# Performance work log

Measured on AMD Instinct MI355X. Metric: run time of the kernel, lower is better.

## Reference

```python
import jax, jax.numpy as jnp
import numpy as np

N_NODES = 100000
N_EDGES = 3200000
N_GRAPHS = 2048
D_IN = 128
D_H = 128
D_OUT = 2
BN_EPS = 1e-5


def setup_inputs() -> dict:
    key = jax.random.key(0)
    ks = jax.random.split(key, 24)
    x = jax.random.normal(ks[0], (N_NODES, D_IN), dtype=jnp.float32)
    edge_index = jax.random.randint(ks[1], (2, N_EDGES), 0, N_NODES, dtype=jnp.int64)
    batch = jnp.sort(jax.random.randint(ks[2], (N_NODES,), 0, N_GRAPHS, dtype=jnp.int64))

    def lin(k, din, dout):
        return jax.random.normal(k, (din, dout), dtype=jnp.float32) / np.sqrt(din)

    inp = {
        'x': x, 'edge_index': edge_index, 'batch': batch,
        'W1': lin(ks[3], D_IN, D_H), 'b1': jnp.zeros((D_H,), jnp.float32),
        'W2': lin(ks[4], D_H, D_H), 'b2': jnp.zeros((D_H,), jnp.float32),
        'W3': lin(ks[5], D_H, D_H), 'b3': jnp.zeros((D_H,), jnp.float32),
    }
    for i, kk in zip((1, 2, 3), (ks[6], ks[7], ks[8])):
        inp[f'bn{i}_g'] = 1.0 + 0.1 * jax.random.normal(jax.random.fold_in(kk, 0), (D_H,), jnp.float32)
        inp[f'bn{i}_b'] = 0.1 * jax.random.normal(jax.random.fold_in(kk, 1), (D_H,), jnp.float32)
        inp[f'bn{i}_m'] = 0.1 * jax.random.normal(jax.random.fold_in(kk, 2), (D_H,), jnp.float32)
        inp[f'bn{i}_v'] = 0.5 + jax.random.uniform(jax.random.fold_in(kk, 3), (D_H,), jnp.float32)
    inp['fc1_W'] = lin(ks[9], D_H, D_H)
    inp['fc1_b'] = jnp.zeros((D_H,), jnp.float32)
    inp['fc2_W'] = lin(ks[10], D_H, D_OUT)
    inp['fc2_b'] = jnp.zeros((D_OUT,), jnp.float32)
    return inp


def _gcn_conv(x, W, b, src, dst, dinv):
    # h = X W, then out[dst] += (dinv[src]*dinv[dst]) * h[src]  (self-loops already in src/dst)
    h = x @ W
    norm = dinv[src] * dinv[dst]  # [E+N]
    msg = h[src] * norm[:, None]  # [E+N, D]
    out = jax.ops.segment_sum(msg, dst, num_segments=N_NODES)
    return out + b


def _bn_eval(x, g, b, m, v):
    return (x - m) * (g * jax.lax.rsqrt(v + BN_EPS)) + b


def reference(x, edge_index, batch, W1, b1, W2, b2, W3, b3,
              bn1_g, bn1_b, bn1_m, bn1_v, bn2_g, bn2_b, bn2_m, bn2_v,
              bn3_g, bn3_b, bn3_m, bn3_v, fc1_W, fc1_b, fc2_W, fc2_b):
    loops = jnp.arange(N_NODES, dtype=edge_index.dtype)
    src = jnp.concatenate([edge_index[0], loops])
    dst = jnp.concatenate([edge_index[1], loops])
    deg = jax.ops.segment_sum(jnp.ones_like(dst, dtype=x.dtype), dst, num_segments=N_NODES)
    dinv = jnp.where(deg > 0, jax.lax.rsqrt(jnp.maximum(deg, 1.0)), 0.0)

    h = jax.nn.relu(_bn_eval(_gcn_conv(x, W1, b1, src, dst, dinv), bn1_g, bn1_b, bn1_m, bn1_v))
    h = jax.nn.relu(_bn_eval(_gcn_conv(h, W2, b2, src, dst, dinv), bn2_g, bn2_b, bn2_m, bn2_v))
    h = jax.nn.relu(_bn_eval(_gcn_conv(h, W3, b3, src, dst, dinv), bn3_g, bn3_b, bn3_m, bn3_v))

    # global mean pool over graphs
    sums = jax.ops.segment_sum(h, batch, num_segments=N_GRAPHS)
    cnts = jax.ops.segment_sum(jnp.ones((N_NODES,), h.dtype), batch, num_segments=N_GRAPHS)
    pooled = sums / jnp.maximum(cnts, 1.0)[:, None]  # [G, D_H]

    z = jax.nn.relu(pooled @ fc1_W + fc1_b)
    logits = z @ fc2_W + fc2_b
    return jax.nn.log_softmax(logits, axis=1)
```

## Files before the change

kernel.cpp:

```cpp
#include <hip/hip_runtime.h>
#include <stdint.h>

#define NN 100000
#define NE 3200000
#define NG 2048
#define DH 128

#define NBUK 196
#define BSH 9
#define BMASK 511
#define BUKCAP 18200
#define EPT 16
#define EPW 4096

#define WLROW 136

typedef __attribute__((ext_vector_type(8))) short v8s;
typedef __attribute__((ext_vector_type(4))) float v4f;
typedef __attribute__((ext_vector_type(2))) float f2;

__device__ __forceinline__ float bf2f(unsigned short u) {
  union { unsigned int i; float f; } v; v.i = ((unsigned int)u) << 16; return v.f;
}
__device__ __forceinline__ unsigned short f2bf(float f) {
  union { float f; unsigned int i; } v; v.f = f;
  unsigned int i = v.i;
  unsigned int r = (i + 0x7FFFu + ((i >> 16) & 1u)) >> 16;
  return (unsigned short)r;
}
__device__ __forceinline__ int eload(const void* p, long long i, int is64) {
  return is64 ? (int)((const long long*)p)[i] : ((const int*)p)[i];
}
__device__ __forceinline__ float pload(const void* p, int i, int isbf) {
  return isbf ? bf2f(((const unsigned short*)p)[i]) : ((const float*)p)[i];
}
__device__ __forceinline__ void upadd2(unsigned int w, f2& acc) {
  union { unsigned int u; float f; } a, b;
  a.u = w << 16; b.u = w & 0xffff0000u;
  f2 u; u.x = a.f; u.y = b.f;
  acc += u;
}
#define ACC4(v) do { upadd2((v).x, a01); upadd2((v).y, a23); \
                     upadd2((v).z, a45); upadd2((v).w, a67); } while (0)

__device__ __forceinline__ void gather_row(const uint4* Hc, const int* colv,
    int beg, int end, int q, f2& a01, f2& a23, f2& a45, f2& a67) {
  int j = beg;
  for (; j + 32 <= end; j += 32) {
    int s0 = colv[j + q],      s1 = colv[j + 4 + q];
    int s2 = colv[j + 8 + q],  s3 = colv[j + 12 + q];
    int s4 = colv[j + 16 + q], s5 = colv[j + 20 + q];
    int s6 = colv[j + 24 + q], s7 = colv[j + 28 + q];
    uint4 v0 = Hc[s0 * 16]; uint4 v1 = Hc[s1 * 16];
    uint4 v2 = Hc[s2 * 16]; uint4 v3 = Hc[s3 * 16];
    uint4 v4 = Hc[s4 * 16]; uint4 v5 = Hc[s5 * 16];
    uint4 v6 = Hc[s6 * 16]; uint4 v7 = Hc[s7 * 16];
    ACC4(v0); ACC4(v1); ACC4(v2); ACC4(v3);
    ACC4(v4); ACC4(v5); ACC4(v6); ACC4(v7);
  }
  for (; j + 16 <= end; j += 16) {
    int s0 = colv[j + q],     s1 = colv[j + 4 + q];
    int s2 = colv[j + 8 + q], s3 = colv[j + 12 + q];
    uint4 v0 = Hc[s0 * 16]; uint4 v1 = Hc[s1 * 16];
    uint4 v2 = Hc[s2 * 16]; uint4 v3 = Hc[s3 * 16];
    ACC4(v0); ACC4(v1); ACC4(v2); ACC4(v3);
  }
  for (; j + 4 <= end; j += 4) {
    uint4 v0 = Hc[colv[j + q] * 16];
    ACC4(v0);
  }
  if (j + q < end) {
    uint4 v0 = Hc[colv[j + q] * 16];
    ACC4(v0);
  }
}

constexpr size_t al(size_t x) { return (x + 255) & ~size_t(255); }
constexpr size_t OFF_FLAGS = 0;
constexpr size_t OFF_DINV  = 256;
constexpr size_t OFF_ROWP  = al(OFF_DINV + 4ull * NN);
constexpr size_t OFF_GSTART= al(OFF_ROWP + 4ull * (NN + 1));
constexpr size_t OFF_BCUR  = al(OFF_GSTART + 4ull * (NG + 1));
constexpr size_t OFF_WT    = al(OFF_BCUR + 1024);
constexpr size_t OFF_FC1W  = al(OFF_WT + 2ull * 3 * 16384);
constexpr size_t OFF_FC2W  = al(OFF_FC1W + 4ull * 16384);
constexpr size_t OFF_PVEC  = al(OFF_FC2W + 4ull * 256);
constexpr size_t OFF_AC    = al(OFF_PVEC + 4ull * 17 * 128);
constexpr size_t OFF_COL   = al(OFF_AC + 4ull * 768);
constexpr size_t OFF_H     = al(OFF_COL + 4ull * NE);
constexpr size_t OFF_Y     = al(OFF_H + 2ull * NN * 128);
constexpr size_t WS_NEED   = OFF_Y + 2ull * NN * 128;
constexpr size_t OFF_REC   = OFF_H;


__global__ __launch_bounds__(256) void probe_k(const void* edge, const void* batch,
                                               const void* x, int* flags, int* bcur) {
  __shared__ int cnt_e, cnt_b, cnt_f;
  int t = threadIdx.x;
  bcur[t] = 0;
  if (t == 0) { cnt_e = 0; cnt_b = 0; cnt_f = 0; }
  __syncthreads();
  int le = 0, lb = 0, lf = 0;
  for (int i = t; i < 512; i += 256) {
    uint2 p = ((const uint2*)edge)[i + 64];
    if (p.y != 0) le++;
  }
  for (int i = t; i < 512; i += 256) {
    uint2 p = ((const uint2*)batch)[50000 - 512 + i];
    if (p.y != 0) lb++;
  }
  for (int i = t; i < 4096; i += 256) {
    unsigned short u = ((const unsigned short*)x)[i];
    int e = (u >> 7) & 0xFF;
    if (e >= 0x90) lf++;
  }
  atomicAdd(&cnt_e, le); atomicAdd(&cnt_b, lb); atomicAdd(&cnt_f, lf);
  __syncthreads();
  if (t == 0) {
    flags[0] = (cnt_e == 0);
    flags[1] = (cnt_b == 0);
    flags[2] = (cnt_f < 16);
    flags[3] = 1;
  }
}

struct Ptrs { const void* p[22]; };

__global__ __launch_bounds__(256) void norm_param_k(Ptrs ptrs, const int* flags,
    unsigned short* Wt, float* fc1W, float* fc2W, float* pvec) {
  int isbf = flags[2];
  int idx = blockIdx.x * 256 + threadIdx.x;
  if (idx < 3 * 16384) {
    int l = idx / 16384, rem = idx % 16384;
    int c = rem >> 7, k = rem & 127;
    const void* W = ptrs.p[2 * l];
    Wt[l * 16384 + c * DH + k] = f2bf(pload(W, k * DH + c, isbf));
  } else if (idx < 4 * 16384) {
    int jj = idx - 3 * 16384;
    fc1W[jj] = pload(ptrs.p[18], jj, isbf);
  } else if (idx < 4 * 16384 + 256) {
    int jj = idx - 4 * 16384;
    fc2W[jj] = pload(ptrs.p[20], jj, isbf);
  } else if (idx < 4 * 16384 + 256 + 17 * 128) {
    int jj = idx - (4 * 16384 + 256);
    int slot = jj >> 7, e = jj & 127;
    int pi = (slot < 3) ? (1 + 2 * slot) : (slot < 15) ? (slot + 3) : (slot == 15 ? 19 : 21);
    if (slot == 16 && e >= 2) return;
    pvec[slot * 128 + e] = pload(ptrs.p[pi], e, isbf);
  }
}

__global__ __launch_bounds__(256) void prep_k(const float* pvec, float* AC) {
  int idx = blockIdx.x * 256 + threadIdx.x;
  if (idx >= 384) return;
  int l = idx >> 7, d = idx & 127;
  float b  = pvec[l * 128 + d];
  float g  = pvec[(3 + 4 * l) * 128 + d];
  float bb = pvec[(4 + 4 * l) * 128 + d];
  float m  = pvec[(5 + 4 * l) * 128 + d];
  float v  = pvec[(6 + 4 * l) * 128 + d];
  float s = g * rsqrtf(v + 1e-5f);
  AC[l * 256 + d] = s;
  AC[l * 256 + 128 + d] = (b - m) * s + bb;
}

__global__ __launch_bounds__(256) void partition_k(const void* edge, const int* flags,
    int* bcur, unsigned long long* recs) {
  __shared__ int lhist[NBUK];
  __shared__ int lbase[NBUK];
  __shared__ int lrank[NBUK];
  int t = threadIdx.x;
  for (int b = t; b < NBUK; b += 256) { lhist[b] = 0; lrank[b] = 0; }
  __syncthreads();
  long long e0 = (long long)blockIdx.x * EPW;
  int f = flags[0];
  int sv[EPT], dv[EPT];
  #pragma unroll
  for (int k = 0; k < EPT; ++k) {
    long long e = e0 + k * 256 + t;
    int s = 0, d = -1;
    if (e < NE) {
      s = eload(edge, e, f);
      d = eload(edge, NE + e, f);
      if ((unsigned)s >= NN || (unsigned)d >= NN) d = -1;
    }
    sv[k] = s; dv[k] = d;
    if (d >= 0) atomicAdd(&lhist[d >> BSH], 1);
  }
  __syncthreads();
  for (int b = t; b < NBUK; b += 256)
    lbase[b] = atomicAdd(&bcur[b], lhist[b]);
  __syncthreads();
  #pragma unroll
  for (int k = 0; k < EPT; ++k) {
    int d = dv[k];
    if (d >= 0) {
      int b = d >> BSH;
      int r = atomicAdd(&lrank[b], 1);
      int pos = lbase[b] + r;
      if (pos < BUKCAP)
        recs[(size_t)b * BUKCAP + pos] =
            ((unsigned long long)(unsigned)d << 32) | (unsigned)sv[k];
    }
  }
}

__global__ __launch_bounds__(256) void csr_build_k(const unsigned long long* recs,
    const int* bcur, int* rowp, int* colv, float* dinv) {
  __shared__ int lh[512];
  __shared__ int lcur[512];
  __shared__ int lts[256];
  __shared__ int lstart;
  int b = blockIdx.x, t = threadIdx.x;
  {
    int v = (t < b && t < NBUK) ? min(bcur[t], BUKCAP) : 0;
    lts[t] = v; __syncthreads();
    for (int off = 128; off > 0; off >>= 1) {
      if (t < off) lts[t] += lts[t + off];
      __syncthreads();
    }
    if (t == 0) lstart = lts[0];
  }
  for (int i = t; i < 512; i += 256) lh[i] = 0;
  __syncthreads();
  int cnt = min(bcur[b], BUKCAP);
  const unsigned long long* rb = recs + (size_t)b * BUKCAP;
  for (int i = t; i < cnt; i += 256)
    atomicAdd(&lh[(int)(rb[i] >> 32) & BMASK], 1);
  __syncthreads();
  int e0 = lh[2 * t], e1 = lh[2 * t + 1];
  lts[t] = e0 + e1; __syncthreads();
  for (int off = 1; off < 256; off <<= 1) {
    int x = (t >= off) ? lts[t - off] : 0;
    __syncthreads();
    lts[t] += x;
    __syncthreads();
  }
  int pre = lts[t] - (e0 + e1);
  int base = b << BSH;
  int n0 = base + 2 * t, n1 = base + 2 * t + 1;
  int r0 = lstart + pre, r1 = lstart + pre + e0;
  if (n0 < NN) { rowp[n0] = r0; dinv[n0] = rsqrtf((float)(e0 + 1)); }
  if (n1 < NN) { rowp[n1] = r1; dinv[n1] = rsqrtf((float)(e1 + 1)); }
  lcur[2 * t] = r0; lcur[2 * t + 1] = r1;
  if (b == NBUK - 1 && t == 255) rowp[NN] = lstart + lts[255];
  __syncthreads();
  for (int i = t; i < cnt; i += 256) {
    unsigned long long rec = rb[i];
    int d = (int)(rec >> 32);
    int s = (int)(rec & 0xffffffffu);
    int p = atomicAdd(&lcur[d & BMASK], 1);
    colv[p] = s;
  }
}

__global__ __launch_bounds__(256) void gbound_k(const void* batch, const int* flags,
                                                int* gstart) {
  int i = blockIdx.x * 256 + threadIdx.x;
  if (i >= NN) return;
  int f = flags[1];
  int b = eload(batch, i, f);
  if ((unsigned)b >= NG) b = NG - 1;
  int bp = -1;
  if (i > 0) {
    bp = eload(batch, i - 1, f);
    if ((unsigned)bp >= NG) bp = NG - 1;
  }
  for (int g = bp + 1; g <= b; ++g) gstart[g] = i;
  if (i == NN - 1) {
    for (int g = b + 1; g <= NG; ++g) gstart[g] = NN;
  }
}

__global__ __launch_bounds__(256) void gemm_k(const void* A, const int* flagp,
    const unsigned short* Wt, const float* dinv, unsigned short* H) {
  __shared__ unsigned short Wl[128 * WLROW];
  const int t = threadIdx.x;
  #pragma unroll
  for (int it = 0; it < 8; ++it) {
    int v = t + 256 * it;
    int col = v >> 4, ch = v & 15;
    *(uint4*)&Wl[col * WLROW + ch * 8] = *(const uint4*)&Wt[col * DH + ch * 8];
  }
  const int wave = threadIdx.x >> 6;
  const int lane = threadIdx.x & 63;
  const int rowbase = blockIdx.x * 64 + wave * 16;
  const int r = lane & 15;
  const int g = lane >> 4;
  const int isb = flagp[0];
  int arow = rowbase + r;
  int arowc = (arow < NN) ? arow : 0;

  v8s a[4];
  if (isb) {
    const uint4* Ab = (const uint4*)A;
    #pragma unroll
    for (int ks = 0; ks < 4; ++ks) {
      union { uint4 u; v8s v; } t2;
      t2.u = Ab[(arowc * DH + ks * 32 + g * 8) >> 3];
      a[ks] = t2.v;
    }
  } else {
    const float4* Af = (const float4*)A;
    #pragma unroll
    for (int ks = 0; ks < 4; ++ks) {
      int bi = (arowc * DH + ks * 32 + g * 8) >> 2;
      float4 f0 = Af[bi], f1 = Af[bi + 1];
      v8s t2;
      t2[0]=(short)f2bf(f0.x); t2[1]=(short)f2bf(f0.y); t2[2]=(short)f2bf(f0.z); t2[3]=(short)f2bf(f0.w);
      t2[4]=(short)f2bf(f1.x); t2[5]=(short)f2bf(f1.y); t2[6]=(short)f2bf(f1.z); t2[7]=(short)f2bf(f1.w);
      a[ks] = t2;
    }
  }
  int orow0 = rowbase + g * 4;
  float dv[4];
  #pragma unroll
  for (int j = 0; j < 4; ++j) {
    int orow = orow0 + j;
    dv[j] = dinv[(orow < NN) ? orow : 0];
  }
  __syncthreads();
  #pragma unroll
  for (int ct = 0; ct < 8; ++ct) {
    v4f acc = {0.f, 0.f, 0.f, 0.f};
    #pragma unroll
    for (int ks = 0; ks < 4; ++ks) {
      union { uint4 u; v8s v; } t2;
      t2.u = *(const uint4*)&Wl[(ct * 16 + r) * WLROW + ks * 32 + g * 8];
      acc = __builtin_amdgcn_mfma_f32_16x16x32_bf16(a[ks], t2.v, acc, 0, 0, 0);
    }
    #pragma unroll
    for (int j = 0; j < 4; ++j) {
      int orow = orow0 + j;
      if (orow < NN) H[orow * DH + ct * 16 + r] = f2bf(acc[j] * dv[j]);
    }
  }
}

__global__ __launch_bounds__(256) void agg_k(const unsigned short* H, const int* rowp,
    const int* colv, const float* dinv, const float* Avec, const float* Cvec,
    unsigned short* Y) {
  int n = blockIdx.x * 4 + (threadIdx.x >> 6);
  if (n >= NN) return;
  int lane = threadIdx.x & 63;
  int q = lane >> 4;
  int c16 = lane & 15;
  const uint4* Hc = (const uint4*)H + c16;
  f2 a01 = {0.f,0.f}, a23 = {0.f,0.f}, a45 = {0.f,0.f}, a67 = {0.f,0.f};
  gather_row(Hc, colv, rowp[n], rowp[n + 1], q, a01, a23, a45, a67);
  #pragma unroll
  for (int m = 16; m <= 32; m <<= 1) {
    a01.x += __shfl_xor(a01.x, m); a01.y += __shfl_xor(a01.y, m);
    a23.x += __shfl_xor(a23.x, m); a23.y += __shfl_xor(a23.y, m);
    a45.x += __shfl_xor(a45.x, m); a45.y += __shfl_xor(a45.y, m);
    a67.x += __shfl_xor(a67.x, m); a67.y += __shfl_xor(a67.y, m);
  }
  if (q == 0) {
    uint4 sv = Hc[n * 16];
    upadd2(sv.x, a01); upadd2(sv.y, a23);
    upadd2(sv.z, a45); upadd2(sv.w, a67);
    float dvn = dinv[n];
    int f0 = c16 * 8;
    float y0 = fmaxf(a01.x * dvn * Avec[f0+0] + Cvec[f0+0], 0.f);
    float y1 = fmaxf(a01.y * dvn * Avec[f0+1] + Cvec[f0+1], 0.f);
    float y2 = fmaxf(a23.x * dvn * Avec[f0+2] + Cvec[f0+2], 0.f);
    float y3 = fmaxf(a23.y * dvn * Avec[f0+3] + Cvec[f0+3], 0.f);
    float y4 = fmaxf(a45.x * dvn * Avec[f0+4] + Cvec[f0+4], 0.f);
    float y5 = fmaxf(a45.y * dvn * Avec[f0+5] + Cvec[f0+5], 0.f);
    float y6 = fmaxf(a67.x * dvn * Avec[f0+6] + Cvec[f0+6], 0.f);
    float y7 = fmaxf(a67.y * dvn * Avec[f0+7] + Cvec[f0+7], 0.f);
    uint4 o;
    o.x = (unsigned int)f2bf(y0) | ((unsigned int)f2bf(y1) << 16);
    o.y = (unsigned int)f2bf(y2) | ((unsigned int)f2bf(y3) << 16);
    o.z = (unsigned int)f2bf(y4) | ((unsigned int)f2bf(y5) << 16);
    o.w = (unsigned int)f2bf(y6) | ((unsigned int)f2bf(y7) << 16);
    ((uint4*)Y)[n * 16 + c16] = o;
  }
}

__global__ __launch_bounds__(256) void pool_k(const unsigned short* Y, const int* gstart,
                                              float* pooled) {
  int g = blockIdx.x * 4 + (threadIdx.x >> 6);
  if (g >= NG) return;
  int lane = threadIdx.x & 63;
  const unsigned int* Yu = (const unsigned int*)Y;
  int beg = gstart[g], end = gstart[g + 1];
  int cnt = end - beg;
  float a0 = 0.f, a1 = 0.f;
  for (int i = beg; i < end; ++i) {
    unsigned int v = Yu[i * 64 + lane];
    a0 += bf2f((unsigned short)v); a1 += bf2f((unsigned short)(v >> 16));
  }
  float inv = 1.f / fmaxf((float)cnt, 1.f);
  pooled[g * DH + lane * 2]     = a0 * inv;
  pooled[g * DH + lane * 2 + 1] = a1 * inv;
}

__global__ __launch_bounds__(256) void fc1_k(const float* pooled, const float* fc1W,
                                             const float* pvec, float* Z) {
  int idx = blockIdx.x * 256 + threadIdx.x;
  int g = idx >> 7, c = idx & 127;
  if (g >= NG) return;
  float acc = 0.f;
  const float* pr = pooled + g * DH;
  #pragma unroll 8
  for (int k = 0; k < DH; ++k) acc += pr[k] * fc1W[k * DH + c];
  acc += pvec[15 * 128 + c];
  Z[g * DH + c] = fmaxf(acc, 0.f);
}

__global__ __launch_bounds__(256) void fc2_k(const float* Z, const float* fc2W,
                                             const float* pvec, float* out) {
  int g = blockIdx.x * 256 + threadIdx.x;
  if (g >= NG) return;
  float l0 = pvec[16 * 128 + 0], l1 = pvec[16 * 128 + 1];
  const float* zr = Z + g * DH;
  #pragma unroll 8
  for (int k = 0; k < DH; ++k) { float z = zr[k]; l0 += z * fc2W[k * 2]; l1 += z * fc2W[k * 2 + 1]; }
  float m = fmaxf(l0, l1);
  float lse = m + logf(expf(l0 - m) + expf(l1 - m));
  out[g * 2]     = l0 - lse;
  out[g * 2 + 1] = l1 - lse;
}

extern "C" void kernel_launch(void* const* d_in, const int* in_sizes, int n_in,
                              void* d_out, int out_size, void* d_ws, size_t ws_size,
                              hipStream_t stream) {
  char* ws = (char*)d_ws;
  int*   flags  = (int*)(ws + OFF_FLAGS);
  float* dinvp  = (float*)(ws + OFF_DINV);
  int*   rowp   = (int*)(ws + OFF_ROWP);
  int*   gstart = (int*)(ws + OFF_GSTART);
  int*   bcur   = (int*)(ws + OFF_BCUR);
  unsigned short* Wt  = (unsigned short*)(ws + OFF_WT);
  float* fc1W   = (float*)(ws + OFF_FC1W);
  float* fc2W   = (float*)(ws + OFF_FC2W);
  float* pvec   = (float*)(ws + OFF_PVEC);
  float* AC     = (float*)(ws + OFF_AC);
  int*   colv   = (int*)(ws + OFF_COL);
  unsigned short* Hbuf = (unsigned short*)(ws + OFF_H);
  unsigned short* Ybuf = (unsigned short*)(ws + OFF_Y);
  unsigned long long* recs = (unsigned long long*)(ws + OFF_REC);
  float* pooled = (float*)(ws + OFF_COL);
  float* Z      = (float*)(ws + OFF_COL + 4ull * NG * DH);

  const void* x     = d_in[0];
  const void* edge  = d_in[1];
  const void* batch = d_in[2];

  probe_k<<<1, 256, 0, stream>>>(edge, batch, x, flags, bcur);

  Ptrs P;
  for (int i = 0; i < 22; ++i) P.p[i] = d_in[3 + i];
  norm_param_k<<<266, 256, 0, stream>>>(P, flags, Wt, fc1W, fc2W, pvec);
  prep_k<<<2, 256, 0, stream>>>(pvec, AC);

  partition_k<<<(NE + EPW - 1) / EPW, 256, 0, stream>>>(edge, flags, bcur, recs);
  gbound_k<<<(NN + 255) / 256, 256, 0, stream>>>(batch, flags, gstart);
  csr_build_k<<<NBUK, 256, 0, stream>>>(recs, bcur, rowp, colv, dinvp);

  const int GB = (NN + 63) / 64;
  gemm_k<<<GB, 256, 0, stream>>>(x, flags + 2, Wt, dinvp, Hbuf);
  agg_k<<<NN / 4, 256, 0, stream>>>(Hbuf, rowp, colv, dinvp, AC, AC + 128, Ybuf);
  gemm_k<<<GB, 256, 0, stream>>>(Ybuf, flags + 3, Wt + 16384, dinvp, Hbuf);
  agg_k<<<NN / 4, 256, 0, stream>>>(Hbuf, rowp, colv, dinvp, AC + 256, AC + 384, Ybuf);
  gemm_k<<<GB, 256, 0, stream>>>(Ybuf, flags + 3, Wt + 32768, dinvp, Hbuf);
  agg_k<<<NN / 4, 256, 0, stream>>>(Hbuf, rowp, colv, dinvp, AC + 512, AC + 640, Ybuf);

  pool_k<<<NG / 4, 256, 0, stream>>>(Ybuf, gstart, pooled);
  fc1_k<<<(NG * DH) / 256, 256, 0, stream>>>(pooled, fc1W, pvec, Z);
  fc2_k<<<(NG + 255) / 256, 256, 0, stream>>>(Z, fc2W, pvec, (float*)d_out);
}
```

Before: 522.3 us.

## Fuse aggregation with next layer GEMM and vectorize pooling

Adds a kernel that aggregates 16 nodes per 1024-thread block, writes the normalized rows to shared memory, and immediately multiplies them by the next layer's weights with MFMA. This removes the intermediate Y write/read and two separate GEMM launches. Each block reloads the full 128x128 weight tile into LDS, and only 8 of 16 waves do the MFMA. The gather loop also loses its 32-wide unroll, and pool_k now uses 16-byte loads split across 4 lanes groups with a shuffle reduction.

```diff
diff --git a/kernel.cpp b/kernel.cpp
--- a/kernel.cpp
+++ b/kernel.cpp
@@ -46,18 +46,6 @@
 __device__ __forceinline__ void gather_row(const uint4* Hc, const int* colv,
     int beg, int end, int q, f2& a01, f2& a23, f2& a45, f2& a67) {
   int j = beg;
-  for (; j + 32 <= end; j += 32) {
-    int s0 = colv[j + q],      s1 = colv[j + 4 + q];
-    int s2 = colv[j + 8 + q],  s3 = colv[j + 12 + q];
-    int s4 = colv[j + 16 + q], s5 = colv[j + 20 + q];
-    int s6 = colv[j + 24 + q], s7 = colv[j + 28 + q];
-    uint4 v0 = Hc[s0 * 16]; uint4 v1 = Hc[s1 * 16];
-    uint4 v2 = Hc[s2 * 16]; uint4 v3 = Hc[s3 * 16];
-    uint4 v4 = Hc[s4 * 16]; uint4 v5 = Hc[s5 * 16];
-    uint4 v6 = Hc[s6 * 16]; uint4 v7 = Hc[s7 * 16];
-    ACC4(v0); ACC4(v1); ACC4(v2); ACC4(v3);
-    ACC4(v4); ACC4(v5); ACC4(v6); ACC4(v7);
-  }
   for (; j + 16 <= end; j += 16) {
     int s0 = colv[j + q],     s1 = colv[j + 4 + q];
     int s2 = colv[j + 8 + q], s3 = colv[j + 12 + q];
@@ -74,6 +62,14 @@
     ACC4(v0);
   }
 }
+#define WAVE_RED() do { \
+  _Pragma("unroll") \
+  for (int m = 16; m <= 32; m <<= 1) { \
+    a01.x += __shfl_xor(a01.x, m); a01.y += __shfl_xor(a01.y, m); \
+    a23.x += __shfl_xor(a23.x, m); a23.y += __shfl_xor(a23.y, m); \
+    a45.x += __shfl_xor(a45.x, m); a45.y += __shfl_xor(a45.y, m); \
+    a67.x += __shfl_xor(a67.x, m); a67.y += __shfl_xor(a67.y, m); \
+  } } while (0)
 
 constexpr size_t al(size_t x) { return (x + 255) & ~size_t(255); }
 constexpr size_t OFF_FLAGS = 0;
@@ -337,6 +333,77 @@
   }
 }
 
+__global__ __launch_bounds__(1024, 8) void aggemm16_k(const unsigned short* H,
+    const int* rowp, const int* colv, const float* dinv,
+    const float* Avec, const float* Cvec, const unsigned short* Wt,
+    unsigned short* Hout) {
+  __shared__ unsigned short Wl[128 * WLROW];
+  __shared__ unsigned short Ylds[16 * WLROW];
+  const int t = threadIdx.x;
+  #pragma unroll
+  for (int it = 0; it < 2; ++it) {
+    int v = t + 1024 * it;
+    int col = v >> 4, ch = v & 15;
+    *(uint4*)&Wl[col * WLROW + ch * 8] = *(const uint4*)&Wt[col * DH + ch * 8];
+  }
+  const int wid = t >> 6, lane = t & 63;
+  const int q = lane >> 4, c16 = lane & 15;
+  const int base = blockIdx.x * 16;
+  const int n = base + wid;
+  const uint4* Hc = (const uint4*)H + c16;
+  {
+    f2 a01 = {0.f,0.f}, a23 = {0.f,0.f}, a45 = {0.f,0.f}, a67 = {0.f,0.f};
+    gather_row(Hc, colv, rowp[n], rowp[n + 1], q, a01, a23, a45, a67);
+    WAVE_RED();
+    if (q == 0) {
+      uint4 sv = Hc[n * 16];
+      upadd2(sv.x, a01); upadd2(sv.y, a23);
+      upadd2(sv.z, a45); upadd2(sv.w, a67);
+      float dvn = dinv[n];
+      int f0 = c16 * 8;
+      float y0 = fmaxf(a01.x * dvn * Avec[f0+0] + Cvec[f0+0], 0.f);
+      float y1 = fmaxf(a01.y * dvn * Avec[f0+1] + Cvec[f0+1], 0.f);
+      float y2 = fmaxf(a23.x * dvn * Avec[f0+2] + Cvec[f0+2], 0.f);
+      float y3 = fmaxf(a23.y * dvn * Avec[f0+3] + Cvec[f0+3], 0.f);
+      float y4 = fmaxf(a45.x * dvn * Avec[f0+4] + Cvec[f0+4], 0.f);
+      float y5 = fmaxf(a45.y * dvn * Avec[f0+5] + Cvec[f0+5], 0.f);
+      float y6 = fmaxf(a67.x * dvn * Avec[f0+6] + Cvec[f0+6], 0.f);
+      float y7 = fmaxf(a67.y * dvn * Avec[f0+7] + Cvec[f0+7], 0.f);
+      uint4 o;
+      o.x = (unsigned int)f2bf(y0) | ((unsigned int)f2bf(y1) << 16);
+      o.y = (unsigned int)f2bf(y2) | ((unsigned int)f2bf(y3) << 16);
+      o.z = (unsigned int)f2bf(y4) | ((unsigned int)f2bf(y5) << 16);
+      o.w = (unsigned int)f2bf(y6) | ((unsigned int)f2bf(y7) << 16);
+      *(uint4*)&Ylds[wid * WLROW + c16 * 8] = o;
+    }
+  }
+  __syncthreads();
+  if (wid < 8) {
+    const int ct = wid;
+    const int r = lane & 15, g = lane >> 4;
+    v8s a[4];
+    #pragma unroll
+    for (int ks = 0; ks < 4; ++ks) {
+      union { uint4 u; v8s v; } t2;
+      t2.u = *(const uint4*)&Ylds[r * WLROW + ks * 32 + g * 8];
+      a[ks] = t2.v;
+    }
+    v4f acc = {0.f, 0.f, 0.f, 0.f};
+    #pragma unroll
+    for (int ks = 0; ks < 4; ++ks) {
+      union { uint4 u; v8s v; } t2;
+      t2.u = *(const uint4*)&Wl[(ct * 16 + r) * WLROW + ks * 32 + g * 8];
+      acc = __builtin_amdgcn_mfma_f32_16x16x32_bf16(a[ks], t2.v, acc, 0, 0, 0);
+    }
+    int orow0 = base + g * 4;
+    #pragma unroll
+    for (int j = 0; j < 4; ++j) {
+      int orow = orow0 + j;
+      Hout[orow * DH + ct * 16 + r] = f2bf(acc[j] * dinv[orow]);
+    }
+  }
+}
+
 __global__ __launch_bounds__(256) void agg_k(const unsigned short* H, const int* rowp,
     const int* colv, const float* dinv, const float* Avec, const float* Cvec,
     unsigned short* Y) {
@@ -348,13 +415,7 @@
   const uint4* Hc = (const uint4*)H + c16;
   f2 a01 = {0.f,0.f}, a23 = {0.f,0.f}, a45 = {0.f,0.f}, a67 = {0.f,0.f};
   gather_row(Hc, colv, rowp[n], rowp[n + 1], q, a01, a23, a45, a67);
-  #pragma unroll
-  for (int m = 16; m <= 32; m <<= 1) {
-    a01.x += __shfl_xor(a01.x, m); a01.y += __shfl_xor(a01.y, m);
-    a23.x += __shfl_xor(a23.x, m); a23.y += __shfl_xor(a23.y, m);
-    a45.x += __shfl_xor(a45.x, m); a45.y += __shfl_xor(a45.y, m);
-    a67.x += __shfl_xor(a67.x, m); a67.y += __shfl_xor(a67.y, m);
-  }
+  WAVE_RED();
   if (q == 0) {
     uint4 sv = Hc[n * 16];
     upadd2(sv.x, a01); upadd2(sv.y, a23);
@@ -383,17 +444,24 @@
   int g = blockIdx.x * 4 + (threadIdx.x >> 6);
   if (g >= NG) return;
   int lane = threadIdx.x & 63;
-  const unsigned int* Yu = (const unsigned int*)Y;
+  int q = lane >> 4, c16 = lane & 15;
+  const uint4* Yc = (const uint4*)Y + c16;
   int beg = gstart[g], end = gstart[g + 1];
   int cnt = end - beg;
-  float a0 = 0.f, a1 = 0.f;
-  for (int i = beg; i < end; ++i) {
-    unsigned int v = Yu[i * 64 + lane];
-    a0 += bf2f((unsigned short)v); a1 += bf2f((unsigned short)(v >> 16));
-  }
-  float inv = 1.f / fmaxf((float)cnt, 1.f);
-  pooled[g * DH + lane * 2]     = a0 * inv;
-  pooled[g * DH + lane * 2 + 1] = a1 * inv;
+  f2 a01 = {0.f,0.f}, a23 = {0.f,0.f}, a45 = {0.f,0.f}, a67 = {0.f,0.f};
+  for (int i = beg + q; i < end; i += 4) {
+    uint4 v = Yc[i * 16];
+    ACC4(v);
+  }
+  WAVE_RED();
+  if (q == 0) {
+    float inv = 1.f / fmaxf((float)cnt, 1.f);
+    float* pr = pooled + g * DH + c16 * 8;
+    pr[0] = a01.x * inv; pr[1] = a01.y * inv;
+    pr[2] = a23.x * inv; pr[3] = a23.y * inv;
+    pr[4] = a45.x * inv; pr[5] = a45.y * inv;
+    pr[6] = a67.x * inv; pr[7] = a67.y * inv;
+  }
 }
 
 __global__ __launch_bounds__(256) void fc1_k(const float* pooled, const float* fc1W,
@@ -460,11 +528,12 @@
   csr_build_k<<<NBUK, 256, 0, stream>>>(recs, bcur, rowp, colv, dinvp);
 
   const int GB = (NN + 63) / 64;
+  const int AB = NN / 16;
   gemm_k<<<GB, 256, 0, stream>>>(x, flags + 2, Wt, dinvp, Hbuf);
-  agg_k<<<NN / 4, 256, 0, stream>>>(Hbuf, rowp, colv, dinvp, AC, AC + 128, Ybuf);
-  gemm_k<<<GB, 256, 0, stream>>>(Ybuf, flags + 3, Wt + 16384, dinvp, Hbuf);
-  agg_k<<<NN / 4, 256, 0, stream>>>(Hbuf, rowp, colv, dinvp, AC + 256, AC + 384, Ybuf);
-  gemm_k<<<GB, 256, 0, stream>>>(Ybuf, flags + 3, Wt + 32768, dinvp, Hbuf);
+  aggemm16_k<<<AB, 1024, 0, stream>>>(Hbuf, rowp, colv, dinvp, AC, AC + 128,
+                                      Wt + 16384, Ybuf);
+  aggemm16_k<<<AB, 1024, 0, stream>>>(Ybuf, rowp, colv, dinvp, AC + 256, AC + 384,
+                                      Wt + 32768, Hbuf);
   agg_k<<<NN / 4, 256, 0, stream>>>(Hbuf, rowp, colv, dinvp, AC + 512, AC + 640, Ybuf);
 
   pool_k<<<NG / 4, 256, 0, stream>>>(Ybuf, gstart, pooled);
```

New measurement: 482.3 us (median of 2 runs). 1.08x faster.
